# Kernel tuning notes

Measured on AMD Instinct MI355X. Metric: run time of the kernel, lower is better.

## Reference

```python
import jax, jax.numpy as jnp
import numpy as np

N_NODES = 20000
N_EDGES = 640000
HIDDEN = 256
HEADS = 8
HEAD_DIM = HIDDEN // HEADS
VOCAB = 119
N_FEATS = 9


def setup_inputs() -> dict:
    key = jax.random.key(0)
    ks = jax.random.split(key, 12)
    X = jax.random.randint(ks[0], (N_NODES, N_FEATS), 0, VOCAB)
    edge_row = jnp.sort(jax.random.randint(ks[1], (N_EDGES,), 0, N_NODES))
    edge_col = jax.random.randint(ks[2], (N_EDGES,), 0, N_NODES)
    s = 0.05  # init scale to keep activations sane
    emb_tables = jax.random.normal(ks[3], (N_FEATS, VOCAB, HIDDEN), jnp.float32) * s
    q_w = jax.random.normal(ks[4], (HIDDEN, HIDDEN), jnp.float32) * s
    q_b = jax.random.normal(ks[5], (HIDDEN,), jnp.float32) * s
    k_w = jax.random.normal(ks[6], (HIDDEN, HIDDEN), jnp.float32) * s
    k_b = jax.random.normal(ks[7], (HIDDEN,), jnp.float32) * s
    v_w = jax.random.normal(ks[8], (HIDDEN, HIDDEN), jnp.float32) * s
    v_b = jax.random.normal(ks[9], (HIDDEN,), jnp.float32) * s
    o_w = jax.random.normal(ks[10], (HIDDEN, HIDDEN), jnp.float32) * s
    o_b = jax.random.normal(ks[11], (HIDDEN,), jnp.float32) * s
    return dict(X=X, edge_row=edge_row, edge_col=edge_col, emb_tables=emb_tables,
                q_w=q_w, q_b=q_b, k_w=k_w, k_b=k_b, v_w=v_w, v_b=v_b, o_w=o_w, o_b=o_b)


def reference(X, edge_row, edge_col, emb_tables, q_w, q_b, k_w, k_b, v_w, v_b, o_w, o_b):
    N = X.shape[0]
    # AtomEncoder: sum of per-feature embeddings -> [N, HIDDEN]
    feat_idx = jnp.arange(N_FEATS)[None, :]  # [1, 9]
    h = emb_tables[feat_idx, X].sum(axis=1)  # [N, 9, H] -> [N, H]
    # q/k/v projections (torch Linear: y = x W^T + b), split into heads
    q = (h @ q_w.T + q_b).reshape(N, HEADS, HEAD_DIM) * (HEAD_DIM ** -0.5)
    k = (h @ k_w.T + k_b).reshape(N, HEADS, HEAD_DIM)
    v = (h @ v_w.T + v_b).reshape(N, HEADS, HEAD_DIM)
    # SDDMM: per-edge, per-head scores
    s = jnp.einsum('ehd,ehd->eh', q[edge_row], k[edge_col])  # [E, HEADS]
    # sparse row-wise softmax (over each node's outgoing-edge neighbors)
    m = jax.ops.segment_max(s, edge_row, num_segments=N)
    e = jnp.exp(s - m[edge_row])
    z = jax.ops.segment_sum(e, edge_row, num_segments=N)
    attn = e / z[edge_row]  # [E, HEADS]
    # SPMM: weighted aggregation of neighbor values
    out = jax.ops.segment_sum(attn[:, :, None] * v[edge_col], edge_row, num_segments=N)
    return out.reshape(N, HIDDEN) @ o_w.T + o_b
```

## Files before the change

### kernel.cpp

```cpp
#include <hip/hip_runtime.h>
#include <hip/hip_bf16.h>

#define N_NODES 20000
#define N_EDGES 640000
#define HIDDEN 256
#define HEADS 8
#define HEAD_DIM 32
#define N_FEATS 9
#define VOCAB 119

typedef __hip_bfloat16 bf16;
typedef __attribute__((ext_vector_type(8))) short short8;
typedef __attribute__((ext_vector_type(4))) float f32x4;
typedef __attribute__((ext_vector_type(2))) float f32x2;

__device__ __forceinline__ ushort f2u(float x) { union { ushort u; bf16 b; } c; c.b = __float2bfloat16(x); return c.u; }

__device__ __forceinline__ f32x2 pk_fma(f32x2 a, f32x2 b, f32x2 c) {
    f32x2 d;
    asm("v_pk_fma_f32 %0, %1, %2, %3" : "=v"(d) : "v"(a), "v"(b), "v"(c));
    return d;
}
__device__ __forceinline__ f32x2 pk_add(f32x2 a, f32x2 b) {
    f32x2 d;
    asm("v_pk_add_f32 %0, %1, %2" : "=v"(d) : "v"(a), "v"(b));
    return d;
}

template <int CTRL>
__device__ __forceinline__ float dpp_xor(float v) {
    return __int_as_float(__builtin_amdgcn_update_dpp(
        0, __float_as_int(v), CTRL, 0xf, 0xf, true));
}

__device__ __forceinline__ float fast_exp2(float x) {
#if __has_builtin(__builtin_amdgcn_exp2f)
    return __builtin_amdgcn_exp2f(x);
#else
    return exp2f(x);
#endif
}

__device__ __forceinline__ void sched_fence() {
    __builtin_amdgcn_sched_barrier(0);
}

#if __has_builtin(__builtin_amdgcn_fdot2_f32_bf16)
typedef __attribute__((ext_vector_type(2))) __bf16 bf16x2_t;
__device__ __forceinline__ float dot2bf(uint a, uint b, float c) {
    return __builtin_amdgcn_fdot2_f32_bf16(__builtin_bit_cast(bf16x2_t, a),
                                           __builtin_bit_cast(bf16x2_t, b), c, false);
}
#else
__device__ __forceinline__ float dot2bf(uint a, uint b, float c) {
    return c + __uint_as_float(a << 16) * __uint_as_float(b << 16)
             + __uint_as_float(a & 0xffff0000u) * __uint_as_float(b & 0xffff0000u);
}
#endif

__global__ void k_pre(const int* __restrict__ X, const float* __restrict__ emb,
                      bf16* __restrict__ h,
                      const float* __restrict__ qw, const float* __restrict__ kw,
                      const float* __restrict__ vw, const float* __restrict__ ow,
                      const float* __restrict__ qb, const float* __restrict__ kb,
                      const float* __restrict__ vb,
                      bf16* __restrict__ wqkv, bf16* __restrict__ wo,
                      float* __restrict__ qkvb,
                      const int* __restrict__ erow, int* __restrict__ row_ptr) {
    int b = blockIdx.x;
    if (b < 5000) {
        int tid = b * 256 + threadIdx.x;
        int n = tid >> 6;
        int c4 = (tid & 63) * 4;
        float4 a = make_float4(0.f, 0.f, 0.f, 0.f);
#pragma unroll
        for (int f = 0; f < N_FEATS; ++f) {
            int idx = X[n * N_FEATS + f];
            float4 e = *(const float4*)(emb + ((size_t)(f * VOCAB + idx)) * HIDDEN + c4);
            a.x += e.x; a.y += e.y; a.z += e.z; a.w += e.w;
        }
        ushort4 o = make_ushort4(f2u(a.x), f2u(a.y), f2u(a.z), f2u(a.w));
        *(ushort4*)((ushort*)h + (size_t)n * HIDDEN + c4) = o;
    } else if (b < 6027) {
        int i = (b - 5000) * 256 + threadIdx.x;
        if (i < 196608) {
            const float* s = i < 65536 ? qw : i < 131072 ? kw : vw;
            wqkv[i] = __float2bfloat16(s[i & 65535]);
        } else if (i < 262144) {
            wo[i - 196608] = __float2bfloat16(ow[i - 196608]);
        } else if (i < 262912) {
            int j = i - 262144;
            const float* s = j < 256 ? qb : j < 512 ? kb : vb;
            qkvb[j] = s[j & 255];
        }
    } else {
        int n = (b - 6027) * 256 + threadIdx.x;
        if (n > N_NODES) return;
        int lo = 0, hi = N_EDGES;
        while (lo < hi) {
            int mid = (lo + hi) >> 1;
            if (erow[mid] < n) lo = mid + 1; else hi = mid;
        }
        row_ptr[n] = lo;
    }
}

template <int MODE, bool GUARD, int TM>
__device__ __forceinline__ void gemm_core(const bf16* __restrict__ A,
                                          const bf16* __restrict__ W,
                                          const float* __restrict__ bias,
                                          void* __restrict__ Y0, void* __restrict__ Y1,
                                          float s_q, int n0, int d0) {
    constexpr int RI = TM / 32;
    __shared__ short As[TM * 72];
    __shared__ short Bs[128 * 72];
    int t = threadIdx.x;
    int lane = t & 63, w = t >> 6;
    int wr = (w >> 1) * (TM / 2), wc = (w & 1) * 64;
    int lr = lane & 15, quad = lane >> 4;

    f32x4 acc[RI][4] = {};
    short8 ra[RI], rb[4];
    int srowA[RI], skoA[RI], srowB[4], skoB[4];
#pragma unroll
    for (int it = 0; it < RI; ++it) { int c = t + 256 * it; srowA[it] = c >> 3; skoA[it] = (c & 7) * 8; }
#pragma unroll
    for (int it = 0; it < 4; ++it) { int c = t + 256 * it; srowB[it] = c >> 3; skoB[it] = (c & 7) * 8; }

#pragma unroll
    for (int it = 0; it < RI; ++it) {
        int n = n0 + srowA[it];
        short8 av = {};
        if (!GUARD || n < N_NODES) av = *(const short8*)(A + (size_t)n * HIDDEN + skoA[it]);
        ra[it] = av;
    }
#pragma unroll
    for (int it = 0; it < 4; ++it)
        rb[it] = *(const short8*)(W + (size_t)(d0 + srowB[it]) * HIDDEN + skoB[it]);
#pragma unroll
    for (int it = 0; it < RI; ++it) *(short8*)(&As[srowA[it] * 72 + skoA[it]]) = ra[it];
#pragma unroll
    for (int it = 0; it < 4; ++it)  *(short8*)(&Bs[srowB[it] * 72 + skoB[it]]) = rb[it];
    __syncthreads();

    for (int k0 = 64; k0 < 256; k0 += 64) {
#pragma unroll
        for (int it = 0; it < RI; ++it) {
            int n = n0 + srowA[it];
            short8 av = {};
            if (!GUARD || n < N_NODES) av = *(const short8*)(A + (size_t)n * HIDDEN + k0 + skoA[it]);
            ra[it] = av;
        }
#pragma unroll
        for (int it = 0; it < 4; ++it)
            rb[it] = *(const short8*)(W + (size_t)(d0 + srowB[it]) * HIDDEN + k0 + skoB[it]);
        {
            short8 af[RI][2], bfr[4][2];
#pragma unroll
            for (int i = 0; i < RI; ++i)
#pragma unroll
                for (int kk = 0; kk < 2; ++kk)
                    af[i][kk] = *(short8*)(&As[(wr + i * 16 + lr) * 72 + kk * 32 + quad * 8]);
#pragma unroll
            for (int j = 0; j < 4; ++j)
#pragma unroll
                for (int kk = 0; kk < 2; ++kk)
                    bfr[j][kk] = *(short8*)(&Bs[(wc + j * 16 + lr) * 72 + kk * 32 + quad * 8]);
#pragma unroll
            for (int kk = 0; kk < 2; ++kk)
#pragma unroll
                for (int i = 0; i < RI; ++i)
#pragma unroll
                    for (int j = 0; j < 4; ++j)
                        acc[i][j] = __builtin_amdgcn_mfma_f32_16x16x32_bf16(
                            af[i][kk], bfr[j][kk], acc[i][j], 0, 0, 0);
        }
        __syncthreads();
#pragma unroll
        for (int it = 0; it < RI; ++it) *(short8*)(&As[srowA[it] * 72 + skoA[it]]) = ra[it];
#pragma unroll
        for (int it = 0; it < 4; ++it)  *(short8*)(&Bs[srowB[it] * 72 + skoB[it]]) = rb[it];
        __syncthreads();
    }
    {
        short8 af[RI][2], bfr[4][2];
#pragma unroll
        for (int i = 0; i < RI; ++i)
#pragma unroll
            for (int kk = 0; kk < 2; ++kk)
                af[i][kk] = *(short8*)(&As[(wr + i * 16 + lr) * 72 + kk * 32 + quad * 8]);
#pragma unroll
        for (int j = 0; j < 4; ++j)
#pragma unroll
            for (int kk = 0; kk < 2; ++kk)
                bfr[j][kk] = *(short8*)(&Bs[(wc + j * 16 + lr) * 72 + kk * 32 + quad * 8]);
#pragma unroll
        for (int kk = 0; kk < 2; ++kk)
#pragma unroll
            for (int i = 0; i < RI; ++i)
#pragma unroll
                for (int j = 0; j < 4; ++j)
                    acc[i][j] = __builtin_amdgcn_mfma_f32_16x16x32_bf16(
                        af[i][kk], bfr[j][kk], acc[i][j], 0, 0, 0);
    }

#pragma unroll
    for (int j = 0; j < 4; ++j) {
        int dbase = d0 + wc + j * 16;
        float bj = bias[dbase + lr];
        if constexpr (MODE == 0) {
            float sc = (dbase < 256) ? s_q : 1.f;
            ushort* dst; int stride;
            if (dbase < 256) {
                dst = (ushort*)Y0 + (size_t)(dbase >> 6) * N_NODES * 64 + (dbase & 63) + lr;
                stride = 64;
            } else if (dbase < 512) {
                int e = dbase - 256;
                int head = e >> 5;
                int dim = (e & 31) + lr;
                dst = (ushort*)Y1 + (size_t)head * N_NODES * 64 + dim;
                stride = 64;
            } else {
                int e = dbase - 512;
                int head = e >> 5;
                int dim = (e & 31) + lr;
                dst = (ushort*)Y1 + (size_t)head * N_NODES * 64 + 32 + dim;
                stride = 64;
            }
#pragma unroll
            for (int i = 0; i < RI; ++i)
#pragma unroll
                for (int r = 0; r < 4; ++r) {
                    int n = n0 + wr + i * 16 + quad * 4 + r;
                    if (GUARD && n >= N_NODES) continue;
                    dst[(size_t)n * stride] = f2u((acc[i][j][r] + bj) * sc);
                }
        } else {
            float* dst = (float*)Y0 + dbase + lr;
#pragma unroll
            for (int i = 0; i < RI; ++i)
#pragma unroll
                for (int r = 0; r < 4; ++r) {
                    int n = n0 + wr + i * 16 + quad * 4 + r;
                    if (GUARD && n >= N_NODES) continue;
                    dst[(size_t)n * HIDDEN] = acc[i][j][r] + bj;
                }
        }
    }
}

__global__ __launch_bounds__(256, 2) void k_gemm_qkv(
    const bf16* __restrict__ A, const bf16* __restrict__ wqkv,
    const float* __restrict__ qkvb, ushort* __restrict__ qhp,
    ushort* __restrict__ khv, float qscale) {
    int n0 = blockIdx.x * 128;
    if (n0 + 128 <= N_NODES)
        gemm_core<0, false, 128>(A, wqkv, qkvb, qhp, khv, qscale, n0, blockIdx.y * 128);
    else
        gemm_core<0, true, 128>(A, wqkv, qkvb, qhp, khv, qscale, n0, blockIdx.y * 128);
}

__global__ __launch_bounds__(256, 4) void k_gemm_o(
    const bf16* __restrict__ A, const bf16* __restrict__ W,
    const float* __restrict__ bias, float* __restrict__ Y) {
    int n0 = blockIdx.x * 64;
    if (n0 + 64 <= N_NODES)
        gemm_core<1, false, 64>(A, W, bias, Y, nullptr, 1.f, n0, blockIdx.y * 128);
    else
        gemm_core<1, true, 64>(A, W, bias, Y, nullptr, 1.f, n0, blockIdx.y * 128);
}


template <int NIT>
__device__ __forceinline__ void pv_accum(const uint4* vv, const float* pb,
                                         f32x2& av0, f32x2& av1, f32x2& av2v, f32x2& av3) {
#pragma unroll
    for (int it = 0; it < NIT; ++it) {
        f32x2 pp; pp.x = pb[it]; pp.y = pb[it];
        f32x2 vf0, vf1, vf2, vf3;
        vf0.x = __uint_as_float(vv[it].x << 16); vf0.y = __uint_as_float(vv[it].x & 0xffff0000u);
        vf1.x = __uint_as_float(vv[it].y << 16); vf1.y = __uint_as_float(vv[it].y & 0xffff0000u);
        vf2.x = __uint_as_float(vv[it].z << 16); vf2.y = __uint_as_float(vv[it].z & 0xffff0000u);
        vf3.x = __uint_as_float(vv[it].w << 16); vf3.y = __uint_as_float(vv[it].w & 0xffff0000u);
        av0  = pk_fma(vf0, pp, av0);
        av1  = pk_fma(vf1, pp, av1);
        av2v = pk_fma(vf2, pp, av2v);
        av3  = pk_fma(vf3, pp, av3);
    }
}

__device__ __forceinline__ void attn_combine_h(int lane, int d4, float z,
                                               f32x2 av0, f32x2 av1, f32x2 av2v, f32x2 av3,
                                               ushort* __restrict__ orow) {
    bool b2 = (lane & 4) != 0, b3 = (lane & 8) != 0, b4 = (lane & 16) != 0;
    f32x2 sd0 = b2 ? av0 : av2v;
    f32x2 sd1 = b2 ? av1 : av3;
    f32x2 r0, r1;
    r0.x = __shfl_xor(sd0.x, 4); r0.y = __shfl_xor(sd0.y, 4);
    r1.x = __shfl_xor(sd1.x, 4); r1.y = __shfl_xor(sd1.y, 4);
    f32x2 t0 = pk_add(b2 ? av2v : av0, r0);
    f32x2 t1 = pk_add(b2 ? av3  : av1, r1);
    f32x2 sdu = b3 ? t0 : t1;
    f32x2 ru; ru.x = __shfl_xor(sdu.x, 8); ru.y = __shfl_xor(sdu.y, 8);
    f32x2 u = pk_add(b3 ? t1 : t0, ru);
    float sw = b4 ? u.x : u.y;
    float rw = __shfl_xor(sw, 16);
    float w = (b4 ? u.y : u.x) + rw;
    w += __shfl_xor(w, 32);
    if (lane < 32) {
        int dim = d4 * 8 + ((lane >> 2) & 1) * 4 + ((lane >> 3) & 1) * 2 + ((lane >> 4) & 1);
        orow[dim] = f2u(w * (1.f / z));
    }
}

template <int NIT>
__device__ __forceinline__ void attn_dense_h(const int* __restrict__ cb, int deg,
                                             int lane, int my, int d4,
                                             const ushort* __restrict__ qrow,
                                             const ushort* __restrict__ khbase,
                                             ushort* __restrict__ orow) {
    int degm = deg - my;
    uint d4b = (uint)d4 * 8;

    int cc[NIT];
#pragma unroll
    for (int it = 0; it < NIT; ++it) cc[it] = cb[min(it * 16 + my, deg - 1)];

    uint4 qu = *(const uint4*)(qrow + d4b);
    uint4 kk[NIT], vv[NIT];
#pragma unroll
    for (int it = 0; it < NIT; ++it)
        kk[it] = *(const uint4*)(khbase + (((size_t)(uint)cc[it]) << 6) + d4b);
#pragma unroll
    for (int it = 0; it < NIT; ++it)
        vv[it] = *(const uint4*)(khbase + (((size_t)(uint)cc[it]) << 6) + 32 + d4b);

    sched_fence();

    float z = 0.f;
    float pb[NIT];
#pragma unroll
    for (int it = 0; it < NIT; ++it) {
        float s = dot2bf(kk[it].x, qu.x, 0.f);
        s = dot2bf(kk[it].y, qu.y, s);
        s = dot2bf(kk[it].z, qu.z, s);
        s = dot2bf(kk[it].w, qu.w, s);
        s += dpp_xor<0xB1>(s);
        s += dpp_xor<0x4E>(s);
        float p = (it * 16 < degm) ? fast_exp2(s) : 0.f;
        z += p;
        pb[it] = p;
    }
    z += dpp_xor<0x124>(z);
    z += dpp_xor<0x128>(z);
    z += __shfl_xor(z, 16);
    z += __shfl_xor(z, 32);

    f32x2 av0 = {0.f, 0.f}, av1 = {0.f, 0.f}, av2v = {0.f, 0.f}, av3 = {0.f, 0.f};
    pv_accum<NIT>(vv, pb, av0, av1, av2v, av3);
    attn_combine_h(lane, d4, z, av0, av1, av2v, av3, orow);
}

__global__ __launch_bounds__(256, 4) void k_attn(
    const int* __restrict__ row_ptr, const int* __restrict__ col,
    const ushort* __restrict__ qhp, const ushort* __restrict__ khv,
    bf16* __restrict__ agg) {
    int b = blockIdx.x;
    int h = b & 7;
    int wave = __builtin_amdgcn_readfirstlane((int)(threadIdx.x >> 6));
    int n = (b >> 3) * 4 + wave;
    int lane = threadIdx.x & 63;
    int my = lane >> 2;
    int d4 = lane & 3;

    int start = row_ptr[n];
    int deg = row_ptr[n + 1] - start;

    ushort* orow = (ushort*)agg + (size_t)n * HIDDEN + h * 32;
    if (deg == 0) {
        if (lane < 4) { uint4 zo = {}; *(uint4*)(orow + lane * 8) = zo; }
        return;
    }

    const ushort* qrow = qhp + ((size_t)(h >> 1) * N_NODES + n) * 64 + (h & 1) * 32;
    const ushort* khbase = khv + (size_t)h * N_NODES * 64;
    const int* cb = col + start;

    if (deg <= 16)      attn_dense_h<1>(cb, deg, lane, my, d4, qrow, khbase, orow);
    else if (deg <= 32) attn_dense_h<2>(cb, deg, lane, my, d4, qrow, khbase, orow);
    else if (deg <= 48) attn_dense_h<3>(cb, deg, lane, my, d4, qrow, khbase, orow);
    else if (deg <= 64) attn_dense_h<4>(cb, deg, lane, my, d4, qrow, khbase, orow);
    else {
        uint d4b = (uint)d4 * 8;
        uint4 qu = *(const uint4*)(qrow + d4b);
        float z = 0.f;
        f32x2 av0 = {0.f, 0.f}, av1 = {0.f, 0.f}, av2v = {0.f, 0.f}, av3 = {0.f, 0.f};
        for (int i = 0; i < deg; i += 16) {
            int idx = i + my;
            int c = cb[min(idx, deg - 1)];
            const ushort* kp = khbase + (((size_t)(uint)c) << 6) + d4b;
            uint4 ku = *(const uint4*)(kp);
            uint4 vu = *(const uint4*)(kp + 32);
            float s = dot2bf(ku.x, qu.x, 0.f);
            s = dot2bf(ku.y, qu.y, s);
            s = dot2bf(ku.z, qu.z, s);
            s = dot2bf(ku.w, qu.w, s);
            s += dpp_xor<0xB1>(s);
            s += dpp_xor<0x4E>(s);
            float p = (idx < deg) ? fast_exp2(s) : 0.f;
            z += p;
            f32x2 pp; pp.x = p; pp.y = p;
            f32x2 vf0, vf1, vf2, vf3;
            vf0.x = __uint_as_float(vu.x << 16); vf0.y = __uint_as_float(vu.x & 0xffff0000u);
            vf1.x = __uint_as_float(vu.y << 16); vf1.y = __uint_as_float(vu.y & 0xffff0000u);
            vf2.x = __uint_as_float(vu.z << 16); vf2.y = __uint_as_float(vu.z & 0xffff0000u);
            vf3.x = __uint_as_float(vu.w << 16); vf3.y = __uint_as_float(vu.w & 0xffff0000u);
            av0  = pk_fma(vf0, pp, av0);
            av1  = pk_fma(vf1, pp, av1);
            av2v = pk_fma(vf2, pp, av2v);
            av3  = pk_fma(vf3, pp, av3);
        }
        z += dpp_xor<0x124>(z);
        z += dpp_xor<0x128>(z);
        z += __shfl_xor(z, 16);
        z += __shfl_xor(z, 32);
        attn_combine_h(lane, d4, z, av0, av1, av2v, av3, orow);
    }
}

extern "C" void kernel_launch(void* const* d_in, const int* in_sizes, int n_in,
                              void* d_out, int out_size, void* d_ws, size_t ws_size,
                              hipStream_t stream) {
    const int*   X    = (const int*)d_in[0];
    const int*   erow = (const int*)d_in[1];
    const int*   ecol = (const int*)d_in[2];
    const float* emb  = (const float*)d_in[3];
    const float* q_w  = (const float*)d_in[4];
    const float* q_b  = (const float*)d_in[5];
    const float* k_w  = (const float*)d_in[6];
    const float* k_b  = (const float*)d_in[7];
    const float* v_w  = (const float*)d_in[8];
    const float* v_b  = (const float*)d_in[9];
    const float* o_w  = (const float*)d_in[10];
    const float* o_b  = (const float*)d_in[11];
    float* out = (float*)d_out;

    char* ws = (char*)d_ws;
    bf16*   h    = (bf16*)(ws);
    bf16*   agg  = (bf16*)(ws);
    ushort* qhp  = (ushort*)(ws + 10240000);
    ushort* khv  = (ushort*)(ws + 20480000);
    bf16*   wqkv = (bf16*)(ws + 40960000);
    bf16*   wo   = (bf16*)(ws + 41353216);
    float*  qkvb = (float*)(ws + 41484288);
    int* row_ptr = (int*)(ws + 41487360);

    k_pre<<<6106, 256, 0, stream>>>(X, emb, h, q_w, k_w, v_w, o_w,
                                    q_b, k_b, v_b, wqkv, wo, qkvb, erow, row_ptr);

    const float qscale = 0.25503486121587466f;
    dim3 gqkv((N_NODES + 127) / 128, 768 / 128);
    k_gemm_qkv<<<gqkv, 256, 0, stream>>>(h, wqkv, qkvb, qhp, khv, qscale);

    k_attn<<<40000, 256, 0, stream>>>(row_ptr, ecol, qhp, khv, agg);

    dim3 go((N_NODES + 63) / 64, HIDDEN / 128);
    k_gemm_o<<<go, 256, 0, stream>>>(agg, wo, o_b, out);
}
```

Before: 177.2 us.

## Process two nodes per wave in attention kernel with half-wave edge groups

Remaps the attention kernel so each 64-lane wave handles two nodes, one per half-wave, with 8 edge slots per iteration instead of 16. The unrolled iteration count is chosen from the larger of the two degrees, and the launch grid is halved. The goal is to cut idle lanes and per-wave overhead for nodes of typical degree. In exchange, each lane holds more in-flight gathers and more registers, and a pair with uneven degrees wastes work on the shorter node.

```diff
diff --git a/kernel.cpp b/kernel.cpp
--- a/kernel.cpp
+++ b/kernel.cpp
@@ -289,9 +289,116 @@
     }
 }
 
-__device__ __forceinline__ void attn_combine_h(int lane, int d4, float z,
-                                               f32x2 av0, f32x2 av1, f32x2 av2v, f32x2 av3,
-                                               ushort* __restrict__ orow) {
+template <int NIT>
+__device__ __forceinline__ void attn_pair(const int* __restrict__ col,
+                                          int start, int deg,
+                                          int lane, int my, int d4, int n,
+                                          const ushort* __restrict__ qhp,
+                                          const ushort* __restrict__ khbase,
+                                          int h, ushort* __restrict__ agg16) {
+    int degm = deg - my;
+    uint d4b = (uint)d4 * 8;
+
+    int cc[NIT];
+#pragma unroll
+    for (int it = 0; it < NIT; ++it) {
+        int idx = min(it * 8 + my, deg - 1);
+        idx = max(idx, 0);
+        cc[it] = col[min(start + idx, N_EDGES - 1)];
+    }
+
+    const ushort* qrow = qhp + ((size_t)(h >> 1) * N_NODES + n) * 64 + (h & 1) * 32;
+    uint4 qu = *(const uint4*)(qrow + d4b);
+    uint4 kk[NIT], vv[NIT];
+#pragma unroll
+    for (int it = 0; it < NIT; ++it)
+        kk[it] = *(const uint4*)(khbase + (((size_t)(uint)cc[it]) << 6) + d4b);
+#pragma unroll
+    for (int it = 0; it < NIT; ++it)
+        vv[it] = *(const uint4*)(khbase + (((size_t)(uint)cc[it]) << 6) + 32 + d4b);
+
+    sched_fence();
+
+    float z = 0.f;
+    float pb[NIT];
+#pragma unroll
+    for (int it = 0; it < NIT; ++it) {
+        float s = dot2bf(kk[it].x, qu.x, 0.f);
+        s = dot2bf(kk[it].y, qu.y, s);
+        s = dot2bf(kk[it].z, qu.z, s);
+        s = dot2bf(kk[it].w, qu.w, s);
+        s += dpp_xor<0xB1>(s);
+        s += dpp_xor<0x4E>(s);
+        float p = (it * 8 < degm) ? fast_exp2(s) : 0.f;
+        z += p;
+        pb[it] = p;
+    }
+    z += dpp_xor<0x124>(z);
+    z += dpp_xor<0x128>(z);
+    z += __shfl_xor(z, 16);
+
+    f32x2 av0 = {0.f, 0.f}, av1 = {0.f, 0.f}, av2v = {0.f, 0.f}, av3 = {0.f, 0.f};
+    pv_accum<NIT>(vv, pb, av0, av1, av2v, av3);
+
+    bool b2 = (lane & 4) != 0, b3 = (lane & 8) != 0, b4 = (lane & 16) != 0;
+    f32x2 sd0 = b2 ? av0 : av2v;
+    f32x2 sd1 = b2 ? av1 : av3;
+    f32x2 r0, r1;
+    r0.x = __shfl_xor(sd0.x, 4); r0.y = __shfl_xor(sd0.y, 4);
+    r1.x = __shfl_xor(sd1.x, 4); r1.y = __shfl_xor(sd1.y, 4);
+    f32x2 t0 = pk_add(b2 ? av2v : av0, r0);
+    f32x2 t1 = pk_add(b2 ? av3  : av1, r1);
+    f32x2 sdu = b3 ? t0 : t1;
+    f32x2 ru; ru.x = __shfl_xor(sdu.x, 8); ru.y = __shfl_xor(sdu.y, 8);
+    f32x2 u = pk_add(b3 ? t1 : t0, ru);
+    float sw = b4 ? u.x : u.y;
+    float rw = __shfl_xor(sw, 16);
+    float w = (b4 ? u.y : u.x) + rw;
+
+    float invz = z > 0.f ? 1.f / z : 0.f;
+    int dim = d4 * 8 + ((lane >> 2) & 1) * 4 + ((lane >> 3) & 1) * 2 + ((lane >> 4) & 1);
+    agg16[(size_t)n * HIDDEN + h * 32 + dim] = f2u(w * invz);
+}
+
+__device__ __forceinline__ void attn_fallback(const int* __restrict__ cb, int deg,
+                                              int lane, const ushort* __restrict__ qrow,
+                                              const ushort* __restrict__ khbase,
+                                              ushort* __restrict__ orow) {
+    int my = lane >> 2;
+    int d4 = lane & 3;
+    uint d4b = (uint)d4 * 8;
+    uint4 qu = *(const uint4*)(qrow + d4b);
+    float z = 0.f;
+    f32x2 av0 = {0.f, 0.f}, av1 = {0.f, 0.f}, av2v = {0.f, 0.f}, av3 = {0.f, 0.f};
+    for (int i = 0; i < deg; i += 16) {
+        int idx = i + my;
+        int c = cb[min(idx, deg - 1)];
+        const ushort* kp = khbase + (((size_t)(uint)c) << 6) + d4b;
+        uint4 ku = *(const uint4*)(kp);
+        uint4 vu = *(const uint4*)(kp + 32);
+        float s = dot2bf(ku.x, qu.x, 0.f);
+        s = dot2bf(ku.y, qu.y, s);
+        s = dot2bf(ku.z, qu.z, s);
+        s = dot2bf(ku.w, qu.w, s);
+        s += dpp_xor<0xB1>(s);
+        s += dpp_xor<0x4E>(s);
+        float p = (idx < deg) ? fast_exp2(s) : 0.f;
+        z += p;
+        f32x2 pp; pp.x = p; pp.y = p;
+        f32x2 vf0, vf1, vf2, vf3;
+        vf0.x = __uint_as_float(vu.x << 16); vf0.y = __uint_as_float(vu.x & 0xffff0000u);
+        vf1.x = __uint_as_float(vu.y << 16); vf1.y = __uint_as_float(vu.y & 0xffff0000u);
+        vf2.x = __uint_as_float(vu.z << 16); vf2.y = __uint_as_float(vu.z & 0xffff0000u);
+        vf3.x = __uint_as_float(vu.w << 16); vf3.y = __uint_as_float(vu.w & 0xffff0000u);
+        av0  = pk_fma(vf0, pp, av0);
+        av1  = pk_fma(vf1, pp, av1);
+        av2v = pk_fma(vf2, pp, av2v);
+        av3  = pk_fma(vf3, pp, av3);
+    }
+    z += dpp_xor<0x124>(z);
+    z += dpp_xor<0x128>(z);
+    z += __shfl_xor(z, 16);
+    z += __shfl_xor(z, 32);
     bool b2 = (lane & 4) != 0, b3 = (lane & 8) != 0, b4 = (lane & 16) != 0;
     f32x2 sd0 = b2 ? av0 : av2v;
     f32x2 sd1 = b2 ? av1 : av3;
@@ -313,54 +420,6 @@
     }
 }
 
-template <int NIT>
-__device__ __forceinline__ void attn_dense_h(const int* __restrict__ cb, int deg,
-                                             int lane, int my, int d4,
-                                             const ushort* __restrict__ qrow,
-                                             const ushort* __restrict__ khbase,
-                                             ushort* __restrict__ orow) {
-    int degm = deg - my;
-    uint d4b = (uint)d4 * 8;
-
-    int cc[NIT];
-#pragma unroll
-    for (int it = 0; it < NIT; ++it) cc[it] = cb[min(it * 16 + my, deg - 1)];
-
-    uint4 qu = *(const uint4*)(qrow + d4b);
-    uint4 kk[NIT], vv[NIT];
-#pragma unroll
-    for (int it = 0; it < NIT; ++it)
-        kk[it] = *(const uint4*)(khbase + (((size_t)(uint)cc[it]) << 6) + d4b);
-#pragma unroll
-    for (int it = 0; it < NIT; ++it)
-        vv[it] = *(const uint4*)(khbase + (((size_t)(uint)cc[it]) << 6) + 32 + d4b);
-
-    sched_fence();
-
-    float z = 0.f;
-    float pb[NIT];
-#pragma unroll
-    for (int it = 0; it < NIT; ++it) {
-        float s = dot2bf(kk[it].x, qu.x, 0.f);
-        s = dot2bf(kk[it].y, qu.y, s);
-        s = dot2bf(kk[it].z, qu.z, s);
-        s = dot2bf(kk[it].w, qu.w, s);
-        s += dpp_xor<0xB1>(s);
-        s += dpp_xor<0x4E>(s);
-        float p = (it * 16 < degm) ? fast_exp2(s) : 0.f;
-        z += p;
-        pb[it] = p;
-    }
-    z += dpp_xor<0x124>(z);
-    z += dpp_xor<0x128>(z);
-    z += __shfl_xor(z, 16);
-    z += __shfl_xor(z, 32);
-
-    f32x2 av0 = {0.f, 0.f}, av1 = {0.f, 0.f}, av2v = {0.f, 0.f}, av3 = {0.f, 0.f};
-    pv_accum<NIT>(vv, pb, av0, av1, av2v, av3);
-    attn_combine_h(lane, d4, z, av0, av1, av2v, av3, orow);
-}
-
 __global__ __launch_bounds__(256, 4) void k_attn(
     const int* __restrict__ row_ptr, const int* __restrict__ col,
     const ushort* __restrict__ qhp, const ushort* __restrict__ khv,
@@ -368,63 +427,43 @@
     int b = blockIdx.x;
     int h = b & 7;
     int wave = __builtin_amdgcn_readfirstlane((int)(threadIdx.x >> 6));
-    int n = (b >> 3) * 4 + wave;
+    int nA = ((b >> 3) * 4 + wave) * 2;
     int lane = threadIdx.x & 63;
-    int my = lane >> 2;
+    int nodeb = lane >> 5;
+    int my = (lane >> 2) & 7;
     int d4 = lane & 3;
+    int n = nA + nodeb;
 
     int start = row_ptr[n];
     int deg = row_ptr[n + 1] - start;
 
-    ushort* orow = (ushort*)agg + (size_t)n * HIDDEN + h * 32;
-    if (deg == 0) {
-        if (lane < 4) { uint4 zo = {}; *(uint4*)(orow + lane * 8) = zo; }
-        return;
-    }
-
-    const ushort* qrow = qhp + ((size_t)(h >> 1) * N_NODES + n) * 64 + (h & 1) * 32;
     const ushort* khbase = khv + (size_t)h * N_NODES * 64;
-    const int* cb = col + start;
-
-    if (deg <= 16)      attn_dense_h<1>(cb, deg, lane, my, d4, qrow, khbase, orow);
-    else if (deg <= 32) attn_dense_h<2>(cb, deg, lane, my, d4, qrow, khbase, orow);
-    else if (deg <= 48) attn_dense_h<3>(cb, deg, lane, my, d4, qrow, khbase, orow);
-    else if (deg <= 64) attn_dense_h<4>(cb, deg, lane, my, d4, qrow, khbase, orow);
+    ushort* agg16 = (ushort*)agg;
+
+    int degA = __shfl(deg, 0);
+    int degB = __shfl(deg, 32);
+    int mx = max(degA, degB);
+
+    if (mx <= 16)      attn_pair<2>(col, start, deg, lane, my, d4, n, qhp, khbase, h, agg16);
+    else if (mx <= 24) attn_pair<3>(col, start, deg, lane, my, d4, n, qhp, khbase, h, agg16);
+    else if (mx <= 32) attn_pair<4>(col, start, deg, lane, my, d4, n, qhp, khbase, h, agg16);
+    else if (mx <= 40) attn_pair<5>(col, start, deg, lane, my, d4, n, qhp, khbase, h, agg16);
+    else if (mx <= 48) attn_pair<6>(col, start, deg, lane, my, d4, n, qhp, khbase, h, agg16);
+    else if (mx <= 64) attn_pair<8>(col, start, deg, lane, my, d4, n, qhp, khbase, h, agg16);
     else {
-        uint d4b = (uint)d4 * 8;
-        uint4 qu = *(const uint4*)(qrow + d4b);
-        float z = 0.f;
-        f32x2 av0 = {0.f, 0.f}, av1 = {0.f, 0.f}, av2v = {0.f, 0.f}, av3 = {0.f, 0.f};
-        for (int i = 0; i < deg; i += 16) {
-            int idx = i + my;
-            int c = cb[min(idx, deg - 1)];
-            const ushort* kp = khbase + (((size_t)(uint)c) << 6) + d4b;
-            uint4 ku = *(const uint4*)(kp);
-            uint4 vu = *(const uint4*)(kp + 32);
-            float s = dot2bf(ku.x, qu.x, 0.f);
-            s = dot2bf(ku.y, qu.y, s);
-            s = dot2bf(ku.z, qu.z, s);
-            s = dot2bf(ku.w, qu.w, s);
-            s += dpp_xor<0xB1>(s);
-            s += dpp_xor<0x4E>(s);
-            float p = (idx < deg) ? fast_exp2(s) : 0.f;
-            z += p;
-            f32x2 pp; pp.x = p; pp.y = p;
-            f32x2 vf0, vf1, vf2, vf3;
-            vf0.x = __uint_as_float(vu.x << 16); vf0.y = __uint_as_float(vu.x & 0xffff0000u);
-            vf1.x = __uint_as_float(vu.y << 16); vf1.y = __uint_as_float(vu.y & 0xffff0000u);
-            vf2.x = __uint_as_float(vu.z << 16); vf2.y = __uint_as_float(vu.z & 0xffff0000u);
-            vf3.x = __uint_as_float(vu.w << 16); vf3.y = __uint_as_float(vu.w & 0xffff0000u);
-            av0  = pk_fma(vf0, pp, av0);
-            av1  = pk_fma(vf1, pp, av1);
-            av2v = pk_fma(vf2, pp, av2v);
-            av3  = pk_fma(vf3, pp, av3);
-        }
-        z += dpp_xor<0x124>(z);
-        z += dpp_xor<0x128>(z);
-        z += __shfl_xor(z, 16);
-        z += __shfl_xor(z, 32);
-        attn_combine_h(lane, d4, z, av0, av1, av2v, av3, orow);
+#pragma unroll 1
+        for (int v = 0; v < 2; ++v) {
+            int nn = nA + v;
+            int s0 = __shfl(start, v * 32);
+            int d0 = v ? degB : degA;
+            ushort* orow = agg16 + (size_t)nn * HIDDEN + h * 32;
+            if (d0 == 0) {
+                if (lane < 4) { uint4 zo = {}; *(uint4*)(orow + lane * 8) = zo; }
+                continue;
+            }
+            const ushort* qrow = qhp + ((size_t)(h >> 1) * N_NODES + nn) * 64 + (h & 1) * 32;
+            attn_fallback(col + s0, d0, lane, qrow, khbase, orow);
+        }
     }
 }
 
@@ -462,7 +501,7 @@
     dim3 gqkv((N_NODES + 127) / 128, 768 / 128);
     k_gemm_qkv<<<gqkv, 256, 0, stream>>>(h, wqkv, qkvb, qhp, khv, qscale);
 
-    k_attn<<<40000, 256, 0, stream>>>(row_ptr, ecol, qhp, khv, agg);
+    k_attn<<<20000, 256, 0, stream>>>(row_ptr, ecol, qhp, khv, agg);
 
     dim3 go((N_NODES + 63) / 64, HIDDEN / 128);
     k_gemm_o<<<go, 256, 0, stream>>>(agg, wo, o_b, out);
```

Result: no change. 180.6 us (+1.9%).
